# Kernel optimization log

Measured on AMD Instinct MI355X. Metric: run time of the kernel, lower is better.

The kernel has to match this reference:

```python
import jax, jax.numpy as jnp
import numpy as np

B, NT, DIM, HEADS = 8, 16, 768, 8
RES_H = RES_W = 32
PIX = RES_H * RES_W              # 1024
CHAN_NH = 16
NH = NW = 4                      # sqrt(chan_nheads)
WH, WW = RES_H // NH, RES_W // NW  # 8, 8
HEAD_DIM = DIM // HEADS          # 96
CHAN_HEAD_DIM = PIX // CHAN_NH   # 64


def _linear(x, w, b=None):
    y = x @ w.T
    return y if b is None else y + b


def _quat_kernel(r, i, j, k):
    # Hamilton-product block kernel: (4*out_c, 4*in_c, K)
    row_r = jnp.concatenate([r, -i, -j, -k], axis=1)
    row_i = jnp.concatenate([i, r, -k, j], axis=1)
    row_j = jnp.concatenate([j, k, r, -i], axis=1)
    row_k = jnp.concatenate([k, -j, i, r], axis=1)
    return jnp.concatenate([row_r, row_i, row_j, row_k], axis=0)


def _conv1d(x, w, b=None, pad=1):
    y = jax.lax.conv_general_dilated(x, w, (1,), [(pad, pad)],
                                     dimension_numbers=('NCH', 'OIH', 'NCH'))
    return y if b is None else y + b[None, :, None]


def _win(z, t):
    # 'b t (nh h nw w) -> b (nh nw) t (h w)'
    b = z.shape[0]
    z = z.reshape(b, t, NH, WH, NW, WW).transpose(0, 2, 4, 1, 3, 5)
    return z.reshape(b, NH * NW, t, WH * WW)


def setup_inputs():
    key = jax.random.key(0)
    ks = jax.random.split(key, 24)
    s = lambda i, shape: jax.random.normal(ks[i], shape, dtype=jnp.float32) * 0.02
    return dict(
        x=jax.random.normal(ks[0], (B, PIX, DIM), jnp.float32),
        task_prompts=jax.random.normal(ks[1], (B, NT, DIM), jnp.float32),
        qkv_w=s(2, (3 * DIM, DIM)),
        proj_w=s(3, (DIM, DIM)), proj_b=s(4, (DIM,)),
        tt_w=s(5, (PIX, DIM)), tt_b=s(6, (PIX,)),
        tt1_w=s(7, (DIM, PIX)), tt1_b=s(8, (DIM,)),
        qf_r=s(9, (2, 1, 3)), qf_i=s(10, (2, 1, 3)), qf_j=s(11, (2, 1, 3)),
        qf_k=s(12, (2, 1, 3)), qf_b=s(13, (8,)),
        dqf_r=s(14, (2, 1, 3)), dqf_i=s(15, (2, 1, 3)), dqf_j=s(16, (2, 1, 3)),
        dqf_k=s(17, (2, 1, 3)), dqf_b=s(18, (4,)),
        bn_g=jnp.ones((4,), jnp.float32), bn_b=jnp.zeros((4,), jnp.float32),
        qfto_w=s(19, (1, 4, 1)),
    )


def reference(x, task_prompts, qkv_w, proj_w, proj_b, tt_w, tt_b, tt1_w, tt1_b,
              qf_r, qf_i, qf_j, qf_k, qf_b, dqf_r, dqf_i, dqf_j, dqf_k, dqf_b,
              bn_g, bn_b, qfto_w):
    # ---- spatial attention over [prompts ; pixels] ----
    xc = jnp.concatenate([task_prompts, x], axis=1)           # (B, N, C), N = NT + PIX
    b, n, c = xc.shape
    qkv = _linear(xc, qkv_w).reshape(b, n, 3, HEADS, HEAD_DIM).transpose(2, 0, 3, 1, 4)
    q, k, v = qkv[0], qkv[1], qkv[2]
    raw_spa = jnp.einsum('bhqd,bhkd->bhqk', q, k)             # pre-scale logits (returned)
    spa_attn = jax.nn.softmax(raw_spa * HEAD_DIM ** -0.5, axis=-1)
    out = jnp.einsum('bhqk,bhkd->bhqd', spa_attn, v).transpose(0, 2, 1, 3).reshape(b, n, c)
    out = _linear(out, proj_w, proj_b)
    tp_out, x_out = out[:, :-PIX, :], out[:, -PIX:, :]        # sep_prompt(x, -pixel_no)

    # ---- windowed channel attention ----
    chan_x = x[:, -PIX:, :]                                   # (B, PIX, C)
    chan_prompts = _linear(task_prompts, tt_w, tt_b)          # (B, NT, PIX)
    qw = _win(chan_prompts, NT)                               # (B, 16, NT, 64)
    kw = _win(chan_x.transpose(0, 2, 1), DIM)                 # (B, 16, C, 64)
    raw_chan = jnp.einsum('bwtd,bwcd->bwtc', qw, kw)          # (B, 16, NT, C)
    chan_attn = jax.nn.softmax(raw_chan * CHAN_HEAD_DIM ** -0.5, axis=-1)
    # chan_x output of attn@v is computed in torch but unused downstream; XLA DCEs it.
    raw_chan_r = raw_chan.reshape(b, NH, NW, NT, DIM).transpose(0, 3, 4, 1, 2)   # b t c nh nw
    chan_attn_r = chan_attn.reshape(b, NH, NW, NT, DIM).transpose(0, 3, 4, 1, 2)

    # ---- quaternion fusion of prompt streams (vectorized over the torch per-sample loop) ----
    ch_prompts = _linear(chan_prompts, tt1_w, tt1_b)          # (B, NT, C)
    zero = jnp.zeros_like(tp_out)
    quater = jnp.stack([zero, task_prompts, tp_out, ch_prompts], axis=2)  # (B, NT, 4, C)
    w1 = _quat_kernel(qf_r, qf_i, qf_j, qf_k)                 # (8, 4, 3), OIH
    fe = _conv1d(quater.reshape(b * NT, 4, DIM), w1, qf_b)    # (B*NT, 8, C)
    w2 = _quat_kernel(dqf_r, dqf_i, dqf_j, dqf_k)             # (8, 4, 3) as (in, out, K)
    w2c = jnp.flip(w2, -1).transpose(1, 0, 2)                 # conv_transpose1d(s=1,p=1) == conv1d(flip, p=K-1-1)
    fe = _conv1d(fe, w2c, dqf_b).reshape(b, NT, 4, DIM)       # (B, NT, 4, C)
    # BatchNorm1d(4) in training mode, stats per loop iteration => per-sample over (NT, C)
    mean = fe.mean(axis=(1, 3), keepdims=True)
    var = fe.var(axis=(1, 3), keepdims=True)
    fe = (fe - mean) / jnp.sqrt(var + 1e-5) * bn_g[None, None, :, None] + bn_b[None, None, :, None]
    fe = jax.nn.gelu(fe, approximate=False)
    quater_out = jnp.einsum('bnkc,k->bnc', fe, qfto_w[0, :, 0])  # Conv1d(4,1,k=1,no bias)
    return (x_out, raw_spa, spa_attn, raw_chan_r, chan_attn_r, quater_out)
```

## Files before the change

kernel.cpp:

```cpp
#include <hip/hip_runtime.h>
#include <hip/hip_bf16.h>
#include <math.h>

typedef unsigned short u16;
typedef __attribute__((ext_vector_type(8))) short  bf16x8;
typedef __attribute__((ext_vector_type(4))) float  f32x4;
typedef __attribute__((ext_vector_type(8))) u16    u16x8;
typedef __attribute__((ext_vector_type(4))) u16    u16x4;

#define B_      8
#define NT_     16
#define DIM_    768
#define HEADS_  8
#define HD_     96
#define PIX_    1024
#define NTOK_   1040
#define NPAD_   1152

#define WSO_XCB     0ull
#define WSO_WQKV    12779520ull
#define WSO_WPROJ   16318464ull
#define WSO_QB      17498112ull
#define WSO_KB      31653888ull
#define WSO_VB      45809664ull
#define WSO_VTB     59965440ull
#define WSO_ACATB   74121216ull
#define WSO_TPB     86900736ull
#define WSO_TTWB    87097344ull
#define WSO_TT1WB   88670208ull
#define WSO_CHANPB  90243072ull
#define WSO_PART    90505216ull
#define WSO_F32     95813632ull
#define FO_TPOUT    0ull
#define FO_RAWCHAN  98304ull
#define FO_CHP      1671168ull
#define FO_FE2      1769472ull
#define FO_STATS    2162688ull

#define OUT_XOUT   0ull
#define OUT_RAW    6291456ull
#define OUT_ATTN   75513856ull
#define OUT_RAWCH  144736256ull
#define OUT_ATTNCH 146309120ull
#define OUT_QOUT   147881984ull

#define SCALE_SPA 0.1020620726159658f

__device__ __forceinline__ u16 f2b(float f) {
    union { float f; unsigned u; } x; x.f = f;
    unsigned r = x.u + 0x7FFFu + ((x.u >> 16) & 1u);
    return (u16)(r >> 16);
}
__device__ __forceinline__ u16 f2b_fast(float f) {
    __hip_bfloat16 h = __float2bfloat16(f);
    return __builtin_bit_cast(u16, h);
}
__device__ __forceinline__ float b2f(u16 h) {
    union { unsigned u; float f; } x; x.u = ((unsigned)h) << 16;
    return x.f;
}

__device__ __forceinline__ void gload_lds16(const u16* gsrc, u16* ldst) {
    __builtin_amdgcn_global_load_lds((const __attribute__((address_space(1))) void*)gsrc,
                                     (__attribute__((address_space(3))) void*)ldst,
                                     16, 0, 0);
}

__global__ __launch_bounds__(256) void cast_concat(const float* __restrict__ tp,
                                                   const float* __restrict__ x,
                                                   u16* __restrict__ xcb) {
    size_t idx8 = ((size_t)blockIdx.x * 256 + threadIdx.x) * 8;
    int c = idx8 % DIM_;
    int n = (idx8 / DIM_) % NTOK_;
    int b = idx8 / ((size_t)DIM_ * NTOK_);
    const float* s = (n < NT_) ? tp + ((size_t)b * NT_ + n) * DIM_ + c
                               : x + ((size_t)b * PIX_ + (n - NT_)) * DIM_ + c;
    float4 a = *(const float4*)s;
    float4 d = *(const float4*)(s + 4);
    u16x8 r;
    r[0] = f2b(a.x); r[1] = f2b(a.y); r[2] = f2b(a.z); r[3] = f2b(a.w);
    r[4] = f2b(d.x); r[5] = f2b(d.y); r[6] = f2b(d.z); r[7] = f2b(d.w);
    *(u16x8*)(xcb + idx8) = r;
}

__global__ __launch_bounds__(256) void cast_all(const float* __restrict__ qkv_w,
                                                const float* __restrict__ proj_w,
                                                const float* __restrict__ tp,
                                                const float* __restrict__ tt_w,
                                                const float* __restrict__ tt1_w,
                                                u16* __restrict__ wqkvb,
                                                u16* __restrict__ wprojb,
                                                u16* __restrict__ tpb,
                                                u16* __restrict__ ttwb,
                                                u16* __restrict__ tt1wb) {
    int i = blockIdx.x * 256 + threadIdx.x;
    const float* src;
    u16* dst;
    int li;
    if (i < 221184)      { src = qkv_w;  dst = wqkvb;  li = i; }
    else if (i < 294912) { src = proj_w; dst = wprojb; li = i - 221184; }
    else if (i < 307200) { src = tp;     dst = tpb;    li = i - 294912; }
    else if (i < 405504) { src = tt_w;   dst = ttwb;   li = i - 307200; }
    else if (i < 503808) { src = tt1_w;  dst = tt1wb;  li = i - 405504; }
    else return;
    const float* s = src + (size_t)li * 8;
    float4 a = *(const float4*)s;
    float4 d = *(const float4*)(s + 4);
    u16x8 r;
    r[0] = f2b(a.x); r[1] = f2b(a.y); r[2] = f2b(a.z); r[3] = f2b(a.w);
    r[4] = f2b(d.x); r[5] = f2b(d.y); r[6] = f2b(d.z); r[7] = f2b(d.w);
    *(u16x8*)(dst + (size_t)li * 8) = r;
}

template <int MODE>
__global__ __launch_bounds__(256) void gemm_bf16(
    const u16* __restrict__ A, const u16* __restrict__ Bw,
    int lda, int ldb, int K, size_t strA, size_t strB,
    const float* __restrict__ bias,
    float* __restrict__ o0, float* __restrict__ o1,
    u16* __restrict__ oq, u16* __restrict__ ok, u16* __restrict__ ov,
    int ldo) {
    __shared__ u16 As[128 * 32];
    __shared__ u16 Bs[128 * 32];
    __shared__ float redm[128][2];
    __shared__ float reds[128][2];
    const int tid = threadIdx.x;
    const int bm = blockIdx.x, bn = blockIdx.y, z = blockIdx.z;
    const u16* Ab = A + strA * z;
    const u16* Bb = Bw + strB * z;
    const int lane = tid & 63, wid = tid >> 6;
    const int ln = lane & 15, hi = lane >> 4;
    const int wr = wid >> 1, wc = wid & 1;
    const int lrow = lane >> 2;
    const int lcol = (lane & 3) * 8;
    f32x4 acc[4][4] = {};
    for (int kt = 0; kt < K; kt += 32) {
        __syncthreads();
#pragma unroll
        for (int t = 0; t < 2; ++t) {
            int rowbase = t * 64 + wid * 16;
            const u16* ga = Ab + (size_t)(bm * 128 + rowbase + lrow) * lda + kt + lcol;
            const u16* gb = Bb + (size_t)(bn * 128 + rowbase + lrow) * ldb + kt + lcol;
            gload_lds16(ga, &As[rowbase * 32]);
            gload_lds16(gb, &Bs[rowbase * 32]);
        }
        __syncthreads();
        bf16x8 af[4], bfr[4];
#pragma unroll
        for (int m = 0; m < 4; ++m)
            af[m] = *(const bf16x8*)&As[(wr * 64 + m * 16 + ln) * 32 + hi * 8];
#pragma unroll
        for (int n = 0; n < 4; ++n)
            bfr[n] = *(const bf16x8*)&Bs[(wc * 64 + n * 16 + ln) * 32 + hi * 8];
#pragma unroll
        for (int m = 0; m < 4; ++m)
#pragma unroll
            for (int n = 0; n < 4; ++n)
                acc[m][n] = __builtin_amdgcn_mfma_f32_16x16x32_bf16(af[m], bfr[n], acc[m][n], 0, 0, 0);
    }
#pragma unroll
    for (int m = 0; m < 4; ++m) {
#pragma unroll
        for (int n = 0; n < 4; ++n) {
#pragma unroll
            for (int j = 0; j < 4; ++j) {
                int gm = bm * 128 + wr * 64 + m * 16 + hi * 4 + j;
                int gn = bn * 128 + wc * 64 + n * 16 + ln;
                float v = acc[m][n][j];
                if (MODE == 0) {
                    int b = gm / NTOK_, nn = gm - b * NTOK_;
                    int s = gn / DIM_, rem = gn - s * DIM_;
                    int h = rem / HD_, d = rem - h * HD_;
                    u16 hv = f2b(v);
                    u16* dst = (s == 0) ? oq : (s == 1) ? ok : ov;
                    dst[(((size_t)b * HEADS_ + h) * NPAD_ + nn) * HD_ + d] = hv;
                } else if (MODE == 1) {
                    if (gm < NTOK_ && gn < NTOK_)
                        __builtin_nontemporal_store(v, &o0[((size_t)z * NTOK_ + gm) * NTOK_ + gn]);
                } else if (MODE == 2) {
                    v += bias[gn];
                    int b = gm / NTOK_, nn = gm - b * NTOK_;
                    if (nn < NT_) o1[((size_t)b * NT_ + nn) * DIM_ + gn] = v;
                    else          __builtin_nontemporal_store(v, &o0[((size_t)b * PIX_ + (nn - NT_)) * DIM_ + gn]);
                } else if (MODE == 3) {
                    oq[(size_t)gm * ldo + gn] = f2b(v + bias[gn]);
                } else {
                    o0[(size_t)gm * ldo + gn] = v + bias[gn];
                }
            }
        }
    }
    if (MODE == 1) {
#pragma unroll
        for (int m = 0; m < 4; ++m) {
#pragma unroll
            for (int j = 0; j < 4; ++j) {
                float v[4];
                float mx = -INFINITY;
#pragma unroll
                for (int n = 0; n < 4; ++n) {
                    int gn = bn * 128 + wc * 64 + n * 16 + ln;
                    v[n] = (gn < NTOK_) ? acc[m][n][j] * SCALE_SPA : -INFINITY;
                    mx = fmaxf(mx, v[n]);
                }
#pragma unroll
                for (int off = 1; off < 16; off <<= 1) mx = fmaxf(mx, __shfl_xor(mx, off));
                float s = 0.f;
                if (mx > -INFINITY) {
#pragma unroll
                    for (int n = 0; n < 4; ++n)
                        if (v[n] > -INFINITY) s += __expf(v[n] - mx);
                }
#pragma unroll
                for (int off = 1; off < 16; off <<= 1) s += __shfl_xor(s, off);
                if (ln == 0) {
                    int row = wr * 64 + m * 16 + hi * 4 + j;
                    redm[row][wc] = mx;
                    reds[row][wc] = s;
                }
            }
        }
        __syncthreads();
        if (tid < 128) {
            float m0 = redm[tid][0], m1 = redm[tid][1];
            float s0 = reds[tid][0], s1 = reds[tid][1];
            float M = fmaxf(m0, m1);
            float S = 0.f;
            if (m0 > -INFINITY) S += s0 * __expf(m0 - M);
            if (m1 > -INFINITY) S += s1 * __expf(m1 - M);
            float2* pp = (float2*)o1;
            pp[((size_t)z * 9 + bn) * NPAD_ + bm * 128 + tid] = make_float2(M, S);
        }
    }
}

__global__ __launch_bounds__(256) void transpose_v(const u16* __restrict__ vb,
                                                   u16* __restrict__ vtb) {
    __shared__ u16 t[32][34];
    int bi = blockIdx.x, bj = blockIdx.y, z = blockIdx.z;
    const u16* ib = vb + (size_t)z * NPAD_ * HD_;
    u16* ob = vtb + (size_t)z * HD_ * NPAD_;
    int tid = threadIdx.x;
    int r = tid >> 3, c = (tid & 7) * 4;
    *(u16x4*)&t[r][c] = *(const u16x4*)(ib + (size_t)(bi * 32 + r) * HD_ + bj * 32 + c);
    __syncthreads();
    u16x4 o;
    o[0] = t[c + 0][r]; o[1] = t[c + 1][r]; o[2] = t[c + 2][r]; o[3] = t[c + 3][r];
    *(u16x4*)(ob + (size_t)(bj * 32 + r) * NPAD_ + bi * 32 + c) = o;
}

__global__ __launch_bounds__(256) void attn_pv4(const float* __restrict__ raw,
                                                const float2* __restrict__ part,
                                                const u16* __restrict__ vtb,
                                                float* __restrict__ attn,
                                                u16* __restrict__ acat) {
    __shared__ u16 Ps[64][136];
    __shared__ float sm[64], si[64];
    const int tid = threadIdx.x;
    const int bi = blockIdx.x, z = blockIdx.y;
    if (tid < 64) {
        int grow = bi * 64 + tid;
        float M = -INFINITY;
        float mj[9], sj[9];
#pragma unroll
        for (int jt = 0; jt < 9; ++jt) {
            float2 p = part[((size_t)z * 9 + jt) * NPAD_ + grow];
            mj[jt] = p.x; sj[jt] = p.y;
            M = fmaxf(M, p.x);
        }
        float S = 0.f;
#pragma unroll
        for (int jt = 0; jt < 9; ++jt)
            if (mj[jt] > -INFINITY) S += sj[jt] * __expf(mj[jt] - M);
        sm[tid] = M;
        si[tid] = 1.f / S;
    }
    __syncthreads();
    const int lane = tid & 63, wid = tid >> 6;
    const int ln = lane & 15, hi = lane >> 4;
    const int wr = wid >> 1, wc = wid & 1;
    const int r0 = tid >> 3, c8 = tid & 7;
    const u16* vbz = vtb + (size_t)z * HD_ * NPAD_;
    const float* rawz = raw + (size_t)z * NTOK_ * NTOK_;
    float* attnz = attn + (size_t)z * NTOK_ * NTOK_;
    int rows[2];
    bool vr[2];
    float mr[2], ir[2];
#pragma unroll
    for (int p = 0; p < 2; ++p) {
        int rr = p * 32 + r0;
        rows[p] = bi * 64 + rr;
        vr[p] = rows[p] < NTOK_;
        mr[p] = sm[rr];
        ir[p] = si[rr];
    }
    f32x4 oacc[2][3] = {};
    for (int c0 = 0; c0 < 1056; c0 += 128) {
        const int nsub = (c0 == 1024) ? 1 : 4;
#pragma unroll 4
        for (int s = 0; s < nsub; ++s) {
            int cl = s * 32 + c8 * 4;
            int col = c0 + cl;
#pragma unroll
            for (int p = 0; p < 2; ++p) {
                int rr = p * 32 + r0;
                bool okc = vr[p] && (col < NTOK_);
                u16x4 pb = {0, 0, 0, 0};
                if (okc) {
                    const float* rp = rawz + (size_t)rows[p] * NTOK_ + col;
                    f32x4 v = __builtin_nontemporal_load((const f32x4*)rp);
                    f32x4 pr;
                    pr[0] = __expf(v[0] * SCALE_SPA - mr[p]) * ir[p];
                    pr[1] = __expf(v[1] * SCALE_SPA - mr[p]) * ir[p];
                    pr[2] = __expf(v[2] * SCALE_SPA - mr[p]) * ir[p];
                    pr[3] = __expf(v[3] * SCALE_SPA - mr[p]) * ir[p];
                    __builtin_nontemporal_store(pr, (f32x4*)(attnz + (size_t)rows[p] * NTOK_ + col));
                    pb[0] = f2b_fast(pr[0]); pb[1] = f2b_fast(pr[1]);
                    pb[2] = f2b_fast(pr[2]); pb[3] = f2b_fast(pr[3]);
                }
                *(u16x4*)&Ps[rr][cl] = pb;
            }
        }
        __syncthreads();
#pragma unroll 4
        for (int ktl = 0; ktl < nsub; ++ktl) {
            bf16x8 af[2];
#pragma unroll
            for (int m = 0; m < 2; ++m)
                af[m] = *(const bf16x8*)&Ps[wr * 32 + m * 16 + ln][ktl * 32 + hi * 8];
#pragma unroll
            for (int n = 0; n < 3; ++n) {
                bf16x8 bv = *(const bf16x8*)(vbz + (size_t)(wc * 48 + n * 16 + ln) * NPAD_
                                             + c0 + ktl * 32 + hi * 8);
#pragma unroll
                for (int m = 0; m < 2; ++m)
                    oacc[m][n] = __builtin_amdgcn_mfma_f32_16x16x32_bf16(af[m], bv, oacc[m][n], 0, 0, 0);
            }
        }
        __syncthreads();
    }
    const int b = z >> 3, h = z & 7;
#pragma unroll
    for (int m = 0; m < 2; ++m)
#pragma unroll
        for (int n = 0; n < 3; ++n)
#pragma unroll
            for (int j = 0; j < 4; ++j) {
                int gi = bi * 64 + wr * 32 + m * 16 + hi * 4 + j;
                if (gi < NTOK_) {
                    int gd = wc * 48 + n * 16 + ln;
                    acat[((size_t)b * NTOK_ + gi) * DIM_ + h * HD_ + gd] = f2b(oacc[m][n][j]);
                }
            }
}

__global__ __launch_bounds__(256) void chan_scores(const u16* __restrict__ chanpb,
                                                   const float* __restrict__ x,
                                                   float* __restrict__ rawchan_ws,
                                                   float* __restrict__ out_raw) {
    int blk = blockIdx.x;
    int b = blk / 16, w = blk % 16;
    int cy = blockIdx.y;
    int nh = w / 4, nw = w % 4;
    __shared__ float qp[16][65];
    __shared__ float xs[64][17];
    int tid = threadIdx.x;
    for (int l = tid; l < 16 * 64; l += 256) {
        int t = l / 64, d = l % 64;
        int wh = d / 8, ww = d % 8;
        int pix = (nh * 8 + wh) * 32 + nw * 8 + ww;
        qp[t][d] = b2f(chanpb[((size_t)b * NT_ + t) * PIX_ + pix]);
    }
    __syncthreads();
    int t = tid % 16, cl = tid / 16;
    for (int cc = cy * 8; cc < cy * 8 + 8; ++cc) {
        for (int l = tid; l < 64 * 16; l += 256) {
            int d = l / 16, c2 = l % 16;
            int wh = d / 8, ww = d % 8;
            int pix = (nh * 8 + wh) * 32 + nw * 8 + ww;
            xs[d][c2] = x[((size_t)b * PIX_ + pix) * DIM_ + cc * 16 + c2];
        }
        __syncthreads();
        float acc = 0.f;
#pragma unroll
        for (int d = 0; d < 64; ++d) acc += qp[t][d] * xs[d][cl];
        int c = cc * 16 + cl;
        rawchan_ws[(((size_t)b * 16 + w) * NT_ + t) * DIM_ + c] = acc;
        out_raw[(((size_t)b * NT_ + t) * DIM_ + c) * 16 + w] = acc;
        __syncthreads();
    }
}

__global__ __launch_bounds__(256) void chan_softmax(const float* __restrict__ rawchan_ws,
                                                    float* __restrict__ out_attn) {
    int row = blockIdx.x;
    int b = row / 256;
    int w = (row / 16) % 16;
    int t = row % 16;
    const float* rp = rawchan_ws + (size_t)row * DIM_;
    int tid = threadIdx.x;
    float vals[3];
    float m = -INFINITY;
#pragma unroll
    for (int i = 0; i < 3; ++i) {
        vals[i] = rp[tid + i * 256] * 0.125f;
        m = fmaxf(m, vals[i]);
    }
    __shared__ float redm[4], reds[4];
    for (int off = 32; off; off >>= 1) m = fmaxf(m, __shfl_xor(m, off));
    if ((tid & 63) == 0) redm[tid >> 6] = m;
    __syncthreads();
    m = fmaxf(fmaxf(redm[0], redm[1]), fmaxf(redm[2], redm[3]));
    float s = 0.f;
#pragma unroll
    for (int i = 0; i < 3; ++i) { vals[i] = __expf(vals[i] - m); s += vals[i]; }
    for (int off = 32; off; off >>= 1) s += __shfl_xor(s, off);
    if ((tid & 63) == 0) reds[tid >> 6] = s;
    __syncthreads();
    s = reds[0] + reds[1] + reds[2] + reds[3];
    float inv = 1.f / s;
#pragma unroll
    for (int i = 0; i < 3; ++i) {
        int c = tid + i * 256;
        out_attn[(((size_t)b * NT_ + t) * DIM_ + c) * 16 + w] = vals[i] * inv;
    }
}

__global__ __launch_bounds__(256) void quat_conv(const float* __restrict__ tp,
                                                 const float* __restrict__ tpo,
                                                 const float* __restrict__ chp,
                                                 const float* __restrict__ qf_r, const float* __restrict__ qf_i,
                                                 const float* __restrict__ qf_j, const float* __restrict__ qf_k,
                                                 const float* __restrict__ qf_b,
                                                 const float* __restrict__ dqf_r, const float* __restrict__ dqf_i,
                                                 const float* __restrict__ dqf_j, const float* __restrict__ dqf_k,
                                                 const float* __restrict__ dqf_b,
                                                 float* __restrict__ fe2_out,
                                                 float* __restrict__ partials) {
    int blk = blockIdx.x;
    int b = blk / NT_, t = blk % NT_;
    __shared__ float w1[8][4][3];
    __shared__ float w2[8][4][3];
    __shared__ float w2c[4][8][3];
    __shared__ float qs[4][770];
    __shared__ float fs[8][770];
    __shared__ float wsum[4][4], wsq[4][4];
    int tid = threadIdx.x;
    if (tid < 96) {
        int o = tid / 12, rest = tid % 12, ic = rest / 3, tap = rest % 3;
        int g = o / 2, oo = o % 2;
        const int   cidx[4][4] = {{0, 1, 2, 3}, {1, 0, 3, 2}, {2, 3, 0, 1}, {3, 2, 1, 0}};
        const float csgn[4][4] = {{1, -1, -1, -1}, {1, 1, -1, 1}, {1, 1, 1, -1}, {1, -1, 1, 1}};
        const float* s1[4] = {qf_r, qf_i, qf_j, qf_k};
        const float* s2[4] = {dqf_r, dqf_i, dqf_j, dqf_k};
        w1[o][ic][tap] = csgn[g][ic] * s1[cidx[g][ic]][oo * 3 + tap];
        w2[o][ic][tap] = csgn[g][ic] * s2[cidx[g][ic]][oo * 3 + tap];
    }
    for (int l = tid; l < DIM_; l += 256) {
        size_t base = ((size_t)b * NT_ + t) * DIM_ + l;
        qs[0][1 + l] = 0.f;
        qs[1][1 + l] = tp[base];
        qs[2][1 + l] = tpo[base];
        qs[3][1 + l] = chp[base];
    }
    if (tid < 4) { qs[tid][0] = 0.f; qs[tid][769] = 0.f; }
    if (tid < 8) { fs[tid][0] = 0.f; fs[tid][769] = 0.f; }
    __syncthreads();
    if (tid < 96) {
        int o2 = tid / 24, rest = tid % 24, i2 = rest / 3, tap = rest % 3;
        w2c[o2][i2][tap] = w2[i2][o2][2 - tap];
    }
    for (int l = tid; l < DIM_; l += 256) {
#pragma unroll
        for (int o = 0; o < 8; ++o) {
            float a = qf_b[o];
#pragma unroll
            for (int ic = 0; ic < 4; ++ic)
#pragma unroll
                for (int tap = 0; tap < 3; ++tap) a += w1[o][ic][tap] * qs[ic][l + tap];
            fs[o][1 + l] = a;
        }
    }
    __syncthreads();
    float lsum[4] = {}, lsq[4] = {};
    for (int l = tid; l < DIM_; l += 256) {
#pragma unroll
        for (int o2 = 0; o2 < 4; ++o2) {
            float a = dqf_b[o2];
#pragma unroll
            for (int i2 = 0; i2 < 8; ++i2)
#pragma unroll
                for (int tap = 0; tap < 3; ++tap) a += w2c[o2][i2][tap] * fs[i2][l + tap];
            fe2_out[((size_t)blk * 4 + o2) * DIM_ + l] = a;
            lsum[o2] += a;
            lsq[o2] += a * a;
        }
    }
    int wid = tid >> 6;
#pragma unroll
    for (int o2 = 0; o2 < 4; ++o2) {
        float s = lsum[o2], q = lsq[o2];
        for (int off = 32; off; off >>= 1) { s += __shfl_xor(s, off); q += __shfl_xor(q, off); }
        if ((tid & 63) == 0) { wsum[wid][o2] = s; wsq[wid][o2] = q; }
    }
    __syncthreads();
    if (tid < 4) {
        float s = wsum[0][tid] + wsum[1][tid] + wsum[2][tid] + wsum[3][tid];
        float q = wsq[0][tid] + wsq[1][tid] + wsq[2][tid] + wsq[3][tid];
        partials[(size_t)blk * 8 + tid * 2 + 0] = s;
        partials[(size_t)blk * 8 + tid * 2 + 1] = q;
    }
}

__global__ __launch_bounds__(256) void bn_gelu_out(const float* __restrict__ fe2,
                                                   const float* __restrict__ partials,
                                                   const float* __restrict__ bn_g,
                                                   const float* __restrict__ bn_b,
                                                   const float* __restrict__ qfto,
                                                   float* __restrict__ out5) {
    int blk = blockIdx.x;
    int b = blk / NT_;
    int tid = threadIdx.x;
    float mean[4], rstd[4], gam[4], bet[4], qw[4];
#pragma unroll
    for (int kk = 0; kk < 4; ++kk) {
        float s = 0.f, q = 0.f;
        for (int t2 = 0; t2 < 16; ++t2) {
            const float* p = partials + ((size_t)(b * NT_ + t2) * 8 + kk * 2);
            s += p[0];
            q += p[1];
        }
        float mu = s * (1.f / 12288.f);
        float var = q * (1.f / 12288.f) - mu * mu;
        mean[kk] = mu;
        rstd[kk] = rsqrtf(var + 1e-5f);
        gam[kk] = bn_g[kk];
        bet[kk] = bn_b[kk];
        qw[kk] = qfto[kk];
    }
    for (int l = tid; l < DIM_; l += 256) {
        float acc = 0.f;
#pragma unroll
        for (int kk = 0; kk < 4; ++kk) {
            float v = fe2[((size_t)blk * 4 + kk) * DIM_ + l];
            float nrm = (v - mean[kk]) * rstd[kk] * gam[kk] + bet[kk];
            float ge = 0.5f * nrm * (1.f + erff(nrm * 0.7071067811865475f));
            acc += ge * qw[kk];
        }
        out5[(size_t)blk * DIM_ + l] = acc;
    }
}

extern "C" void kernel_launch(void* const* d_in, const int* in_sizes, int n_in,
                              void* d_out, int out_size, void* d_ws, size_t ws_size,
                              hipStream_t stream) {
    const float* x      = (const float*)d_in[0];
    const float* tp     = (const float*)d_in[1];
    const float* qkv_w  = (const float*)d_in[2];
    const float* proj_w = (const float*)d_in[3];
    const float* proj_b = (const float*)d_in[4];
    const float* tt_w   = (const float*)d_in[5];
    const float* tt_b   = (const float*)d_in[6];
    const float* tt1_w  = (const float*)d_in[7];
    const float* tt1_b  = (const float*)d_in[8];
    const float* qf_r   = (const float*)d_in[9];
    const float* qf_i   = (const float*)d_in[10];
    const float* qf_j   = (const float*)d_in[11];
    const float* qf_k   = (const float*)d_in[12];
    const float* qf_b   = (const float*)d_in[13];
    const float* dqf_r  = (const float*)d_in[14];
    const float* dqf_i  = (const float*)d_in[15];
    const float* dqf_j  = (const float*)d_in[16];
    const float* dqf_k  = (const float*)d_in[17];
    const float* dqf_b  = (const float*)d_in[18];
    const float* bn_g   = (const float*)d_in[19];
    const float* bn_b   = (const float*)d_in[20];
    const float* qfto   = (const float*)d_in[21];
    float* out = (float*)d_out;
    char* wsb = (char*)d_ws;

    u16* xcb    = (u16*)(wsb + WSO_XCB);
    u16* wqkvb  = (u16*)(wsb + WSO_WQKV);
    u16* wprojb = (u16*)(wsb + WSO_WPROJ);
    u16* qb     = (u16*)(wsb + WSO_QB);
    u16* kb     = (u16*)(wsb + WSO_KB);
    u16* vb     = (u16*)(wsb + WSO_VB);
    u16* vtb    = (u16*)(wsb + WSO_VTB);
    u16* acatb  = (u16*)(wsb + WSO_ACATB);
    u16* tpb    = (u16*)(wsb + WSO_TPB);
    u16* ttwb   = (u16*)(wsb + WSO_TTWB);
    u16* tt1wb  = (u16*)(wsb + WSO_TT1WB);
    u16* chanpb = (u16*)(wsb + WSO_CHANPB);
    float* partb = (float*)(wsb + WSO_PART);
    float* f32r = (float*)(wsb + WSO_F32);
    float* tpout   = f32r + FO_TPOUT;
    float* rawchan = f32r + FO_RAWCHAN;
    float* chpf    = f32r + FO_CHP;
    float* fe2     = f32r + FO_FE2;
    float* stats   = f32r + FO_STATS;

    cast_concat<<<3120, 256, 0, stream>>>(tp, x, xcb);
    cast_all<<<1968, 256, 0, stream>>>(qkv_w, proj_w, tp, tt_w, tt1_w,
                                       wqkvb, wprojb, tpb, ttwb, tt1wb);

    gemm_bf16<0><<<dim3(65, 18, 1), 256, 0, stream>>>(xcb, wqkvb, 768, 768, 768, 0, 0,
                                                      nullptr, nullptr, nullptr, qb, kb, vb, 0);
    transpose_v<<<dim3(36, 3, 64), 256, 0, stream>>>(vb, vtb);
    gemm_bf16<1><<<dim3(9, 9, 64), 256, 0, stream>>>(qb, kb, 96, 96, 96,
                                                     (size_t)NPAD_ * HD_, (size_t)NPAD_ * HD_,
                                                     nullptr, out + OUT_RAW, partb,
                                                     nullptr, nullptr, nullptr, 0);
    attn_pv4<<<dim3(17, 64), 256, 0, stream>>>(out + OUT_RAW, (const float2*)partb,
                                               vtb, out + OUT_ATTN, acatb);
    gemm_bf16<2><<<dim3(65, 6, 1), 256, 0, stream>>>(acatb, wprojb, 768, 768, 768, 0, 0,
                                                     proj_b, out + OUT_XOUT, tpout,
                                                     nullptr, nullptr, nullptr, 0);
    gemm_bf16<3><<<dim3(1, 8, 1), 256, 0, stream>>>(tpb, ttwb, 768, 768, 768, 0, 0,
                                                    tt_b, nullptr, nullptr, chanpb, nullptr, nullptr, 1024);
    chan_scores<<<dim3(128, 6), 256, 0, stream>>>(chanpb, x, rawchan, out + OUT_RAWCH);
    chan_softmax<<<2048, 256, 0, stream>>>(rawchan, out + OUT_ATTNCH);
    gemm_bf16<4><<<dim3(1, 6, 1), 256, 0, stream>>>(chanpb, tt1wb, 1024, 1024, 1024, 0, 0,
                                                    tt1_b, chpf, nullptr, nullptr, nullptr, nullptr, 768);
    quat_conv<<<128, 256, 0, stream>>>(tp, tpout, chpf,
                                       qf_r, qf_i, qf_j, qf_k, qf_b,
                                       dqf_r, dqf_i, dqf_j, dqf_k, dqf_b,
                                       fe2, stats);
    bn_gelu_out<<<128, 256, 0, stream>>>(fe2, stats, bn_g, bn_b, qfto, out + OUT_QOUT);
}
```

Before: 498.7 us.

## Fuse cast kernels and enlarge attention PV row tile to 128

Merges the two fp32-to-bf16 cast kernels into one launch to drop one kernel launch. The softmax-normalize + PV kernel now processes 128 query rows per block instead of 64, so each V fragment loaded from global memory feeds four MFMA row tiles instead of two. Blocks drop from 17 to 9 per head, which lowers V reloads but raises register and LDS use and reduces the number of blocks available to fill the GPU.

New measurement: 506.6 us. About the same (+1.6%).

```diff
diff --git a/kernel.cpp b/kernel.cpp
--- a/kernel.cpp
+++ b/kernel.cpp
@@ -66,50 +66,49 @@
                                      16, 0, 0);
 }
 
-__global__ __launch_bounds__(256) void cast_concat(const float* __restrict__ tp,
-                                                   const float* __restrict__ x,
-                                                   u16* __restrict__ xcb) {
-    size_t idx8 = ((size_t)blockIdx.x * 256 + threadIdx.x) * 8;
-    int c = idx8 % DIM_;
-    int n = (idx8 / DIM_) % NTOK_;
-    int b = idx8 / ((size_t)DIM_ * NTOK_);
-    const float* s = (n < NT_) ? tp + ((size_t)b * NT_ + n) * DIM_ + c
-                               : x + ((size_t)b * PIX_ + (n - NT_)) * DIM_ + c;
+__global__ __launch_bounds__(256) void cast_fused(const float* __restrict__ tp,
+                                                  const float* __restrict__ x,
+                                                  const float* __restrict__ qkv_w,
+                                                  const float* __restrict__ proj_w,
+                                                  const float* __restrict__ tt_w,
+                                                  const float* __restrict__ tt1_w,
+                                                  u16* __restrict__ xcb,
+                                                  u16* __restrict__ wqkvb,
+                                                  u16* __restrict__ wprojb,
+                                                  u16* __restrict__ tpb,
+                                                  u16* __restrict__ ttwb,
+                                                  u16* __restrict__ tt1wb) {
+    int bx = blockIdx.x, tid = threadIdx.x;
+    const float* s;
+    u16* d8;
+    if (bx < 3120) {
+        size_t idx8 = ((size_t)bx * 256 + tid) * 8;
+        int c = idx8 % DIM_;
+        int n = (idx8 / DIM_) % NTOK_;
+        int b = idx8 / ((size_t)DIM_ * NTOK_);
+        s = (n < NT_) ? tp + ((size_t)b * NT_ + n) * DIM_ + c
+                      : x + ((size_t)b * PIX_ + (n - NT_)) * DIM_ + c;
+        d8 = xcb + idx8;
+    } else {
+        int i = (bx - 3120) * 256 + tid;
+        const float* src;
+        u16* dst;
+        int li;
+        if (i < 221184)      { src = qkv_w;  dst = wqkvb;  li = i; }
+        else if (i < 294912) { src = proj_w; dst = wprojb; li = i - 221184; }
+        else if (i < 307200) { src = tp;     dst = tpb;    li = i - 294912; }
+        else if (i < 405504) { src = tt_w;   dst = ttwb;   li = i - 307200; }
+        else if (i < 503808) { src = tt1_w;  dst = tt1wb;  li = i - 405504; }
+        else return;
+        s = src + (size_t)li * 8;
+        d8 = dst + (size_t)li * 8;
+    }
     float4 a = *(const float4*)s;
     float4 d = *(const float4*)(s + 4);
     u16x8 r;
     r[0] = f2b(a.x); r[1] = f2b(a.y); r[2] = f2b(a.z); r[3] = f2b(a.w);
     r[4] = f2b(d.x); r[5] = f2b(d.y); r[6] = f2b(d.z); r[7] = f2b(d.w);
-    *(u16x8*)(xcb + idx8) = r;
-}
-
-__global__ __launch_bounds__(256) void cast_all(const float* __restrict__ qkv_w,
-                                                const float* __restrict__ proj_w,
-                                                const float* __restrict__ tp,
-                                                const float* __restrict__ tt_w,
-                                                const float* __restrict__ tt1_w,
-                                                u16* __restrict__ wqkvb,
-                                                u16* __restrict__ wprojb,
-                                                u16* __restrict__ tpb,
-                                                u16* __restrict__ ttwb,
-                                                u16* __restrict__ tt1wb) {
-    int i = blockIdx.x * 256 + threadIdx.x;
-    const float* src;
-    u16* dst;
-    int li;
-    if (i < 221184)      { src = qkv_w;  dst = wqkvb;  li = i; }
-    else if (i < 294912) { src = proj_w; dst = wprojb; li = i - 221184; }
-    else if (i < 307200) { src = tp;     dst = tpb;    li = i - 294912; }
-    else if (i < 405504) { src = tt_w;   dst = ttwb;   li = i - 307200; }
-    else if (i < 503808) { src = tt1_w;  dst = tt1wb;  li = i - 405504; }
-    else return;
-    const float* s = src + (size_t)li * 8;
-    float4 a = *(const float4*)s;
-    float4 d = *(const float4*)(s + 4);
-    u16x8 r;
-    r[0] = f2b(a.x); r[1] = f2b(a.y); r[2] = f2b(a.z); r[3] = f2b(a.w);
-    r[4] = f2b(d.x); r[5] = f2b(d.y); r[6] = f2b(d.z); r[7] = f2b(d.w);
-    *(u16x8*)(dst + (size_t)li * 8) = r;
+    *(u16x8*)d8 = r;
 }
 
 template <int MODE>
@@ -249,17 +248,17 @@
     *(u16x4*)(ob + (size_t)(bj * 32 + r) * NPAD_ + bi * 32 + c) = o;
 }
 
-__global__ __launch_bounds__(256) void attn_pv4(const float* __restrict__ raw,
+__global__ __launch_bounds__(256) void attn_pv5(const float* __restrict__ raw,
                                                 const float2* __restrict__ part,
                                                 const u16* __restrict__ vtb,
                                                 float* __restrict__ attn,
                                                 u16* __restrict__ acat) {
-    __shared__ u16 Ps[64][136];
-    __shared__ float sm[64], si[64];
+    __shared__ u16 Ps[128][136];
+    __shared__ float sm[128], si[128];
     const int tid = threadIdx.x;
     const int bi = blockIdx.x, z = blockIdx.y;
-    if (tid < 64) {
-        int grow = bi * 64 + tid;
+    if (tid < 128) {
+        int grow = bi * 128 + tid;
         float M = -INFINITY;
         float mj[9], sj[9];
 #pragma unroll
@@ -283,18 +282,18 @@
     const u16* vbz = vtb + (size_t)z * HD_ * NPAD_;
     const float* rawz = raw + (size_t)z * NTOK_ * NTOK_;
     float* attnz = attn + (size_t)z * NTOK_ * NTOK_;
-    int rows[2];
-    bool vr[2];
-    float mr[2], ir[2];
-#pragma unroll
-    for (int p = 0; p < 2; ++p) {
+    int rows[4];
+    bool vr[4];
+    float mr[4], ir[4];
+#pragma unroll
+    for (int p = 0; p < 4; ++p) {
         int rr = p * 32 + r0;
-        rows[p] = bi * 64 + rr;
+        rows[p] = bi * 128 + rr;
         vr[p] = rows[p] < NTOK_;
         mr[p] = sm[rr];
         ir[p] = si[rr];
     }
-    f32x4 oacc[2][3] = {};
+    f32x4 oacc[4][3] = {};
     for (int c0 = 0; c0 < 1056; c0 += 128) {
         const int nsub = (c0 == 1024) ? 1 : 4;
 #pragma unroll 4
@@ -302,7 +301,7 @@
             int cl = s * 32 + c8 * 4;
             int col = c0 + cl;
 #pragma unroll
-            for (int p = 0; p < 2; ++p) {
+            for (int p = 0; p < 4; ++p) {
                 int rr = p * 32 + r0;
                 bool okc = vr[p] && (col < NTOK_);
                 u16x4 pb = {0, 0, 0, 0};
@@ -324,16 +323,16 @@
         __syncthreads();
 #pragma unroll 4
         for (int ktl = 0; ktl < nsub; ++ktl) {
-            bf16x8 af[2];
-#pragma unroll
-            for (int m = 0; m < 2; ++m)
-                af[m] = *(const bf16x8*)&Ps[wr * 32 + m * 16 + ln][ktl * 32 + hi * 8];
+            bf16x8 af[4];
+#pragma unroll
+            for (int m = 0; m < 4; ++m)
+                af[m] = *(const bf16x8*)&Ps[wr * 64 + m * 16 + ln][ktl * 32 + hi * 8];
 #pragma unroll
             for (int n = 0; n < 3; ++n) {
                 bf16x8 bv = *(const bf16x8*)(vbz + (size_t)(wc * 48 + n * 16 + ln) * NPAD_
                                              + c0 + ktl * 32 + hi * 8);
 #pragma unroll
-                for (int m = 0; m < 2; ++m)
+                for (int m = 0; m < 4; ++m)
                     oacc[m][n] = __builtin_amdgcn_mfma_f32_16x16x32_bf16(af[m], bv, oacc[m][n], 0, 0, 0);
             }
         }
@@ -341,12 +340,12 @@
     }
     const int b = z >> 3, h = z & 7;
 #pragma unroll
-    for (int m = 0; m < 2; ++m)
+    for (int m = 0; m < 4; ++m)
 #pragma unroll
         for (int n = 0; n < 3; ++n)
 #pragma unroll
             for (int j = 0; j < 4; ++j) {
-                int gi = bi * 64 + wr * 32 + m * 16 + hi * 4 + j;
+                int gi = bi * 128 + wr * 64 + m * 16 + hi * 4 + j;
                 if (gi < NTOK_) {
                     int gd = wc * 48 + n * 16 + ln;
                     acat[((size_t)b * NTOK_ + gi) * DIM_ + h * HD_ + gd] = f2b(oacc[m][n][j]);
@@ -599,9 +598,8 @@
     float* fe2     = f32r + FO_FE2;
     float* stats   = f32r + FO_STATS;
 
-    cast_concat<<<3120, 256, 0, stream>>>(tp, x, xcb);
-    cast_all<<<1968, 256, 0, stream>>>(qkv_w, proj_w, tp, tt_w, tt1_w,
-                                       wqkvb, wprojb, tpb, ttwb, tt1wb);
+    cast_fused<<<5088, 256, 0, stream>>>(tp, x, qkv_w, proj_w, tt_w, tt1_w,
+                                         xcb, wqkvb, wprojb, tpb, ttwb, tt1wb);
 
     gemm_bf16<0><<<dim3(65, 18, 1), 256, 0, stream>>>(xcb, wqkvb, 768, 768, 768, 0, 0,
                                                       nullptr, nullptr, nullptr, qb, kb, vb, 0);
@@ -610,8 +608,8 @@
                                                      (size_t)NPAD_ * HD_, (size_t)NPAD_ * HD_,
                                                      nullptr, out + OUT_RAW, partb,
                                                      nullptr, nullptr, nullptr, 0);
-    attn_pv4<<<dim3(17, 64), 256, 0, stream>>>(out + OUT_RAW, (const float2*)partb,
-                                               vtb, out + OUT_ATTN, acatb);
+    attn_pv5<<<dim3(9, 64), 256, 0, stream>>>(out + OUT_RAW, (const float2*)partb,
+                                              vtb, out + OUT_ATTN, acatb);
     gemm_bf16<2><<<dim3(65, 6, 1), 256, 0, stream>>>(acatb, wprojb, 768, 768, 768, 0, 0,
                                                      proj_b, out + OUT_XOUT, tpout,
                                                      nullptr, nullptr, nullptr, 0);
```
